# Kernel tuning notes

Measured on AMD Instinct MI355X. Metric: run time of the kernel, lower is better.

The kernel has to match this reference:

```python
import jax, jax.numpy as jnp
import numpy as np

N_NODES = 50000
N_EDGES = 800000


def gcn_layer(x, edge_index, W, b):
    """PyG-style GCNConv: add self-loops, symmetric deg^-1/2 normalization,
    linear transform, scatter-sum aggregation at target nodes, plus bias."""
    n = x.shape[0]
    loops = jnp.arange(n)
    src = jnp.concatenate([edge_index[0], loops])  # [E+N]
    dst = jnp.concatenate([edge_index[1], loops])  # [E+N]
    deg = jax.ops.segment_sum(jnp.ones(src.shape, dtype=x.dtype), dst, num_segments=n)
    dinv = jnp.where(deg > 0, jax.lax.rsqrt(deg), jnp.zeros((), x.dtype))
    norm = dinv[src] * dinv[dst]               # [E+N]
    h = x @ W                                   # [N, out]
    msg = norm[:, None] * h[src]                # [E+N, out] gather
    out = jax.ops.segment_sum(msg, dst, num_segments=n)  # scatter-add
    return out + b


def setup_inputs() -> dict:
    key = jax.random.key(0)
    ks = jax.random.split(key, 8)
    features = jax.random.normal(ks[0], (N_NODES, 64), dtype=jnp.float32)
    edge_index1 = jax.random.randint(ks[1], (2, N_EDGES), 0, N_NODES)
    edge_index3 = jax.random.randint(ks[2], (2, N_EDGES), 0, N_NODES)
    edge_index9 = jax.random.randint(ks[3], (2, N_EDGES), 0, N_NODES)

    def glorot(k, fi, fo):
        lim = float(np.sqrt(6.0 / (fi + fo)))
        return jax.random.uniform(k, (fi, fo), minval=-lim, maxval=lim, dtype=jnp.float32)

    W1 = glorot(ks[4], 64, 64)
    W2 = glorot(ks[5], 64, 32)
    W3 = glorot(ks[6], 32, 16)
    b1 = jnp.zeros((64,), jnp.float32)
    b2 = jnp.zeros((32,), jnp.float32)
    b3 = jnp.zeros((16,), jnp.float32)
    return dict(features=features, edge_index1=edge_index1, edge_index3=edge_index3,
                edge_index9=edge_index9, W1=W1, b1=b1, W2=W2, b2=b2, W3=W3, b3=b3)


def reference(features, edge_index1, edge_index3, edge_index9, W1, b1, W2, b2, W3, b3):
    x = jax.nn.relu(gcn_layer(features, edge_index1, W1, b1))  # hop 1
    x = jax.nn.relu(gcn_layer(x, edge_index3, W2, b2))         # hop 3
    x = jax.nn.relu(gcn_layer(x, edge_index9, W3, b3))         # hop 9
    return x
```

## Files before the change

kernel.cpp:

```cpp
#include <hip/hip_runtime.h>
#include <hip/hip_fp16.h>


#define NB   256
#define NL   3
#define TB   (NB * NL)
#define CAPE 6400
#define CAPE_E (CAPE + 8)
#define CH   4096
#define P1T  256
#define EPT  (CH / P1T)
#define P2T  512

__device__ __forceinline__ void decode_chunk(int g, int nc1, int nc2,
                                             const int* s1, const int* d1, int E1,
                                             const int* s2, const int* d2, int E2,
                                             const int* s3, const int* d3, int E3,
                                             const int** src, const int** dst, int* E, int* l,
                                             int* gout) {
    if (g < nc1)            { *src = s1; *dst = d1; *E = E1; *l = 0; }
    else if (g < nc1 + nc2) { *src = s2; *dst = d2; *E = E2; *l = 1; g -= nc1; }
    else                    { *src = s3; *dst = d3; *E = E3; *l = 2; g -= nc1 + nc2; }
    *gout = g;
}

__device__ __forceinline__ void fma4(float4& a, float s, const float4& w) {
    a.x += s * w.x; a.y += s * w.y; a.z += s * w.z; a.w += s * w.w;
}
__device__ __forceinline__ void add4(float4& a, const float4& v) {
    a.x += v.x; a.y += v.y; a.z += v.z; a.w += v.w;
}
__device__ __forceinline__ float4 ldh4(const __half* h, size_t idx4) {
    uint2 r = ((const uint2*)h)[idx4];
    __half2 a = *reinterpret_cast<__half2*>(&r.x);
    __half2 b = *reinterpret_cast<__half2*>(&r.y);
    float2 fa = __half22float2(a), fb = __half22float2(b);
    return make_float4(fa.x, fa.y, fb.x, fb.y);
}
__device__ __forceinline__ void sth4(__half* h, size_t idx4, float4 v) {
    __half2 a = __floats2half2_rn(v.x, v.y);
    __half2 b = __floats2half2_rn(v.z, v.w);
    uint2 r;
    r.x = *reinterpret_cast<unsigned*>(&a);
    r.y = *reinterpret_cast<unsigned*>(&b);
    ((uint2*)h)[idx4] = r;
}

__device__ __forceinline__ int wave_incl_scan(int v) {
    int incl = v;
#pragma unroll
    for (int off = 1; off < 64; off <<= 1) {
        int u = __shfl_up(incl, (unsigned)off, 64);
        if ((threadIdx.x & 63) >= off) incl += u;
    }
    return incl;
}

__global__ void __launch_bounds__(P1T) k1_phase1_gemm1(
        const int* __restrict__ s1, const int* __restrict__ d1, int E1,
        const int* __restrict__ s2, const int* __restrict__ d2, int E2,
        const int* __restrict__ s3, const int* __restrict__ d3, int E3,
        int nc1, int nc2, int W, int nchunks,
        int* __restrict__ gcur, unsigned int* __restrict__ pairBuf,
        const float* __restrict__ x0, const float* __restrict__ W1g,
        __half* __restrict__ h1) {
    __shared__ __align__(16) char smem[24576];
    __shared__ int wsum[4];
    const int t = threadIdx.x;
    if (blockIdx.x < (unsigned)nchunks) {
        int* hist = (int*)smem;
        int* eofs = hist + NB;
        int* bo   = eofs + NB;
        int* lcur = bo + NB;
        unsigned* stage = (unsigned*)(smem + 4096);
        unsigned char* stageQ = (unsigned char*)(smem + 20480);
        hist[t] = 0;
        __syncthreads();
        const int* src; const int* dst; int E, l, g;
        decode_chunk(blockIdx.x, nc1, nc2, s1, d1, E1, s2, d2, E2, s3, d3, E3,
                     &src, &dst, &E, &l, &g);
        const int e0 = g * CH;
        const int lbase = l * NB;
        unsigned pv[EPT];
        int bn[EPT];
        if (E - e0 >= CH) {
            const int4* s4 = (const int4*)(src + e0);
            const int4* d4 = (const int4*)(dst + e0);
#pragma unroll
            for (int w = 0; w < EPT / 4; ++w) {
                int4 sv = s4[t + w * P1T];
                int4 dv = d4[t + w * P1T];
                int q, i = w * 4;
                q = dv.x / W; bn[i+0] = q; pv[i+0] = ((unsigned)sv.x << 9) | (unsigned)(dv.x - q * W);
                q = dv.y / W; bn[i+1] = q; pv[i+1] = ((unsigned)sv.y << 9) | (unsigned)(dv.y - q * W);
                q = dv.z / W; bn[i+2] = q; pv[i+2] = ((unsigned)sv.z << 9) | (unsigned)(dv.z - q * W);
                q = dv.w / W; bn[i+3] = q; pv[i+3] = ((unsigned)sv.w << 9) | (unsigned)(dv.w - q * W);
            }
        } else {
#pragma unroll
            for (int i = 0; i < EPT; ++i) {
                int e = e0 + t + i * P1T;
                if (e < E) {
                    int s = src[e], d = dst[e];
                    int q = d / W;
                    bn[i] = q;
                    pv[i] = ((unsigned)s << 9) | (unsigned)(d - q * W);
                } else bn[i] = -1;
            }
        }
#pragma unroll
        for (int i = 0; i < EPT; ++i)
            if (bn[i] >= 0) atomicAdd(&hist[bn[i]], 1);
        __syncthreads();
        const int c = hist[t];
        int incl = wave_incl_scan(c);
        const int lane = t & 63, wid = t >> 6;
        if (lane == 63) wsum[wid] = incl;
        __syncthreads();
        int base = 0, total = 0;
#pragma unroll
        for (int w = 0; w < 4; ++w) {
            int s = wsum[w];
            total += s;
            if (w < wid) base += s;
        }
        const int excl = base + incl - c;
        eofs[t] = excl;
        lcur[t] = excl;
        bo[t] = (lbase + t) * CAPE + (c ? atomicAdd(&gcur[lbase + t], c) : 0);
        __syncthreads();
#pragma unroll
        for (int i = 0; i < EPT; ++i) {
            if (bn[i] >= 0) {
                int r = atomicAdd(&lcur[bn[i]], 1);
                stage[r] = pv[i];
                stageQ[r] = (unsigned char)bn[i];
            }
        }
        __syncthreads();
        for (int i = t; i < total; i += P1T) {
            int q = stageQ[i];
            int k = bo[q] + (i - eofs[q]);
            if (k < (lbase + q + 1) * CAPE) pairBuf[k] = stage[i];
        }
    } else {
        float* Ws = (float*)smem;
        const int bid = blockIdx.x - nchunks;
        for (int i = t; i < 1024; i += P1T)
            ((float4*)Ws)[i] = ((const float4*)W1g)[i];
        __syncthreads();
        const int tc = t % 16;
        const int tr = t / 16;
        const int row0 = bid * 64 + tr * 4;
        const float4* x4 = (const float4*)x0;
        const float4* Ws4 = (const float4*)Ws;
        float4 acc[4];
#pragma unroll
        for (int r = 0; r < 4; ++r) acc[r] = make_float4(0.f, 0.f, 0.f, 0.f);
        int rowc[4];
#pragma unroll
        for (int r = 0; r < 4; ++r) rowc[r] = min(row0 + r, 49999);
        for (int k0 = 0; k0 < 64; k0 += 4) {
            float4 wv0 = Ws4[(k0 + 0) * 16 + tc];
            float4 wv1 = Ws4[(k0 + 1) * 16 + tc];
            float4 wv2 = Ws4[(k0 + 2) * 16 + tc];
            float4 wv3 = Ws4[(k0 + 3) * 16 + tc];
#pragma unroll
            for (int r = 0; r < 4; ++r) {
                float4 xv = x4[(size_t)rowc[r] * 16 + (k0 / 4)];
                fma4(acc[r], xv.x, wv0);
                fma4(acc[r], xv.y, wv1);
                fma4(acc[r], xv.z, wv2);
                fma4(acc[r], xv.w, wv3);
            }
        }
#pragma unroll
        for (int r = 0; r < 4; ++r) {
            int row = row0 + r;
            if (row < 50000) sth4(h1, (size_t)row * 16 + tc, acc[r]);
        }
    }
}

__global__ void __launch_bounds__(P2T) k2_phase2(
        const unsigned int* __restrict__ pairBuf, const int* __restrict__ gcur,
        int n, int W,
        int* __restrict__ row_ptr, int* __restrict__ cnt_g,
        float* __restrict__ dinv, unsigned short* __restrict__ eidx,
        __half* __restrict__ h1, int* __restrict__ perm) {
    __shared__ __align__(16) char smem[19456];
    __shared__ int wsum[8];
    int* lcnt  = (int*)smem;
    int* lscan = lcnt + P2T;
    unsigned short* stage = (unsigned short*)(lscan + P2T);
    float* dloc = (float*)(smem + 17408);
    const int bid = blockIdx.x;
    const int l = bid / NB, k = bid % NB;
    const int lo = k * W;
    const int hi = min(n, lo + W);
    const int Wn = hi - lo;
    const int segE = min(gcur[bid], CAPE);
    const size_t base  = (size_t)bid * CAPE;
    const int    baseE = bid * CAPE_E;
    const int t = threadIdx.x;
    const int lane = t & 63, wid = t >> 6;
    lcnt[t] = 0;
    __syncthreads();
    for (int i = t; i < segE; i += P2T)
        atomicAdd(&lcnt[pairBuf[base + i] & 511u], 1);
    __syncthreads();
    const int v = lcnt[t];
    const int vp = (v + 3) & ~3;
    int incl = wave_incl_scan(vp);
    if (lane == 63) wsum[wid] = incl;
    __syncthreads();
    int sbase = 0, segEp = 0;
#pragma unroll
    for (int w = 0; w < 8; ++w) {
        int s = wsum[w];
        segEp += s;
        if (w < wid) sbase += s;
    }
    const int pexcl = sbase + incl - vp;
    if (t < Wn) {
        int node = l * n + lo + t;
        row_ptr[node] = baseE + pexcl;
        cnt_g[node] = v;
        float dv = rsqrtf((float)v + 1.0f);
        dinv[node] = dv;
        dloc[t] = dv;
    }
    __syncthreads();
    lcnt[t] = pexcl;
    __syncthreads();
    const bool lds_ok = (segEp <= CAPE);
    for (int i = t; i < segE; i += P2T) {
        unsigned p = pairBuf[base + i];
        int pos = atomicAdd(&lcnt[p & 511u], 1);
        unsigned short s = (unsigned short)(p >> 9);
        if (lds_ok) stage[pos] = s;
        else if (pos < CAPE_E) eidx[baseE + pos] = s;
    }
    __syncthreads();
    if (lds_ok) {
        const int4* st4 = (const int4*)stage;
        int4* e4 = (int4*)(eidx + baseE);
        int m16 = (segEp + 7) >> 3;
        for (int i = t; i < m16; i += P2T) e4[i] = st4[i];
    }
    if (l == 0) {
        for (int i = t; i < Wn * 16; i += P2T) {
            int r = i >> 4, cc = i & 15;
            size_t idx = (size_t)(lo + r) * 16 + cc;
            float4 vv = ldh4(h1, idx);
            float s = dloc[r];
            vv.x *= s; vv.y *= s; vv.z *= s; vv.w *= s;
            sth4(h1, idx, vv);
        }
    }
    __syncthreads();
    lcnt[t] = 0;
    __syncthreads();
    int key = 0, myr = 0;
    if (t < Wn) {
        key = min(v, 511);
        myr = atomicAdd(&lcnt[key], 1);
    }
    __syncthreads();
    const int c2 = lcnt[t];
    int incl2 = wave_incl_scan(c2);
    if (lane == 63) wsum[wid] = incl2;
    __syncthreads();
    int base2 = 0;
#pragma unroll
    for (int w = 0; w < 8; ++w) {
        int s = wsum[w];
        if (w < wid) base2 += s;
    }
    lscan[t] = base2 + incl2 - c2;
    __syncthreads();
    if (t < Wn) perm[l * n + lo + lscan[key] + myr] = lo + t;
}

__global__ void __launch_bounds__(256) k3_gather1_gemm2(
        const int* __restrict__ row_ptr, const int* __restrict__ cnt,
        const unsigned short* __restrict__ eidx, const float* __restrict__ dinv1,
        const float* __restrict__ dinv2, const int* __restrict__ perm,
        const __half* __restrict__ h1, const float* __restrict__ b1,
        const float* __restrict__ W2g, __half* __restrict__ h2, int n) {
    __shared__ float xs[16 * 68];
    __shared__ float W2s[64 * 32];
    for (int i = threadIdx.x; i < 512; i += 256)
        ((float4*)W2s)[i] = ((const float4*)W2g)[i];
    const int ln = threadIdx.x >> 4;
    const int f4 = threadIdx.x & 15;
    const int gidx = blockIdx.x * 16 + ln;
    const int node = (gidx < n) ? perm[gidx] : 0;
    if (gidx < n) {
        const int beg = row_ptr[node];
        const int m = cnt[node];
        float4 a0 = make_float4(0.f, 0.f, 0.f, 0.f), a1 = a0, a2 = a0, a3 = a0;
        int j = 0;
        for (; j + 8 <= m; j += 8) {
            ushort4 e0 = *(const ushort4*)(eidx + beg + j);
            ushort4 e1 = *(const ushort4*)(eidx + beg + j + 4);
            add4(a0, ldh4(h1, (size_t)e0.x * 16 + f4));
            add4(a1, ldh4(h1, (size_t)e0.y * 16 + f4));
            add4(a2, ldh4(h1, (size_t)e0.z * 16 + f4));
            add4(a3, ldh4(h1, (size_t)e0.w * 16 + f4));
            add4(a0, ldh4(h1, (size_t)e1.x * 16 + f4));
            add4(a1, ldh4(h1, (size_t)e1.y * 16 + f4));
            add4(a2, ldh4(h1, (size_t)e1.z * 16 + f4));
            add4(a3, ldh4(h1, (size_t)e1.w * 16 + f4));
        }
        if (j + 4 <= m) {
            ushort4 e0 = *(const ushort4*)(eidx + beg + j);
            add4(a0, ldh4(h1, (size_t)e0.x * 16 + f4));
            add4(a1, ldh4(h1, (size_t)e0.y * 16 + f4));
            add4(a2, ldh4(h1, (size_t)e0.z * 16 + f4));
            add4(a3, ldh4(h1, (size_t)e0.w * 16 + f4));
            j += 4;
        }
        for (; j < m; ++j)
            add4(a0, ldh4(h1, (size_t)eidx[beg + j] * 16 + f4));
        add4(a0, a1); add4(a2, a3); add4(a0, a2);
        float di = dinv1[node];
        float4 self = ldh4(h1, (size_t)node * 16 + f4);
        float4 bv = ((const float4*)b1)[f4];
        float4 o;
        o.x = di * (a0.x + self.x) + bv.x;
        o.y = di * (a0.y + self.y) + bv.y;
        o.z = di * (a0.z + self.z) + bv.z;
        o.w = di * (a0.w + self.w) + bv.w;
        o.x = o.x > 0.f ? o.x : 0.f;
        o.y = o.y > 0.f ? o.y : 0.f;
        o.z = o.z > 0.f ? o.z : 0.f;
        o.w = o.w > 0.f ? o.w : 0.f;
        *(float4*)&xs[ln * 68 + f4 * 4] = o;
    }
    __syncthreads();
    if (gidx < n) {
        const int c0 = f4 * 2;
        float s0 = 0.f, s1 = 0.f;
#pragma unroll
        for (int k = 0; k < 64; ++k) {
            float xv = xs[ln * 68 + k];
            s0 += xv * W2s[k * 32 + c0];
            s1 += xv * W2s[k * 32 + c0 + 1];
        }
        float d2 = dinv2[node];
        ((__half2*)h2)[(size_t)node * 16 + f4] = __floats2half2_rn(s0 * d2, s1 * d2);
    }
}

__global__ void __launch_bounds__(256) k4_gather2_gemm3(
        const int* __restrict__ row_ptr2, const int* __restrict__ cnt2,
        const unsigned short* __restrict__ eidx, const float* __restrict__ dinv2,
        const float* __restrict__ dinv3, const int* __restrict__ perm,
        const __half* __restrict__ h2, const float* __restrict__ b2,
        const float* __restrict__ W3g, __half* __restrict__ h3, int n) {
    __shared__ float xs[32 * 36];
    __shared__ float W3s[32 * 16];
    for (int i = threadIdx.x; i < 128; i += 256)
        ((float4*)W3s)[i] = ((const float4*)W3g)[i];
    const int ln = threadIdx.x >> 3;
    const int f4 = threadIdx.x & 7;
    const int gidx = blockIdx.x * 32 + ln;
    const int node = (gidx < n) ? perm[gidx] : 0;
    if (gidx < n) {
        const int beg = row_ptr2[node];
        const int m = cnt2[node];
        float4 a0 = make_float4(0.f, 0.f, 0.f, 0.f), a1 = a0, a2 = a0, a3 = a0;
        int j = 0;
        for (; j + 8 <= m; j += 8) {
            ushort4 e0 = *(const ushort4*)(eidx + beg + j);
            ushort4 e1 = *(const ushort4*)(eidx + beg + j + 4);
            add4(a0, ldh4(h2, (size_t)e0.x * 8 + f4));
            add4(a1, ldh4(h2, (size_t)e0.y * 8 + f4));
            add4(a2, ldh4(h2, (size_t)e0.z * 8 + f4));
            add4(a3, ldh4(h2, (size_t)e0.w * 8 + f4));
            add4(a0, ldh4(h2, (size_t)e1.x * 8 + f4));
            add4(a1, ldh4(h2, (size_t)e1.y * 8 + f4));
            add4(a2, ldh4(h2, (size_t)e1.z * 8 + f4));
            add4(a3, ldh4(h2, (size_t)e1.w * 8 + f4));
        }
        if (j + 4 <= m) {
            ushort4 e0 = *(const ushort4*)(eidx + beg + j);
            add4(a0, ldh4(h2, (size_t)e0.x * 8 + f4));
            add4(a1, ldh4(h2, (size_t)e0.y * 8 + f4));
            add4(a2, ldh4(h2, (size_t)e0.z * 8 + f4));
            add4(a3, ldh4(h2, (size_t)e0.w * 8 + f4));
            j += 4;
        }
        for (; j < m; ++j)
            add4(a0, ldh4(h2, (size_t)eidx[beg + j] * 8 + f4));
        add4(a0, a1); add4(a2, a3); add4(a0, a2);
        float di = dinv2[node];
        float4 self = ldh4(h2, (size_t)node * 8 + f4);
        float4 bv = ((const float4*)b2)[f4];
        float4 o;
        o.x = di * (a0.x + self.x) + bv.x;
        o.y = di * (a0.y + self.y) + bv.y;
        o.z = di * (a0.z + self.z) + bv.z;
        o.w = di * (a0.w + self.w) + bv.w;
        o.x = o.x > 0.f ? o.x : 0.f;
        o.y = o.y > 0.f ? o.y : 0.f;
        o.z = o.z > 0.f ? o.z : 0.f;
        o.w = o.w > 0.f ? o.w : 0.f;
        *(float4*)&xs[ln * 36 + f4 * 4] = o;
    }
    __syncthreads();
    if (gidx < n) {
        const int c0 = f4 * 2;
        float s0 = 0.f, s1 = 0.f;
#pragma unroll
        for (int k = 0; k < 32; ++k) {
            float xv = xs[ln * 36 + k];
            s0 += xv * W3s[k * 16 + c0];
            s1 += xv * W3s[k * 16 + c0 + 1];
        }
        float d3 = dinv3[node];
        ((__half2*)h3)[(size_t)node * 8 + f4] = __floats2half2_rn(s0 * d3, s1 * d3);
    }
}

__global__ void __launch_bounds__(256) k5_gather3(
        const int* __restrict__ row_ptr3, const int* __restrict__ cnt3,
        const unsigned short* __restrict__ eidx, const float* __restrict__ dinv3,
        const int* __restrict__ perm,
        const __half* __restrict__ h3, const float* __restrict__ b3,
        float* __restrict__ out, int n) {
    const int ln = threadIdx.x >> 2;
    const int f4 = threadIdx.x & 3;
    const int gidx = blockIdx.x * 64 + ln;
    if (gidx >= n) return;
    const int node = perm[gidx];
    const int beg = row_ptr3[node];
    const int m = cnt3[node];
    float4 a0 = make_float4(0.f, 0.f, 0.f, 0.f), a1 = a0, a2 = a0, a3 = a0;
    int j = 0;
    for (; j + 8 <= m; j += 8) {
        ushort4 e0 = *(const ushort4*)(eidx + beg + j);
        ushort4 e1 = *(const ushort4*)(eidx + beg + j + 4);
        add4(a0, ldh4(h3, (size_t)e0.x * 4 + f4));
        add4(a1, ldh4(h3, (size_t)e0.y * 4 + f4));
        add4(a2, ldh4(h3, (size_t)e0.z * 4 + f4));
        add4(a3, ldh4(h3, (size_t)e0.w * 4 + f4));
        add4(a0, ldh4(h3, (size_t)e1.x * 4 + f4));
        add4(a1, ldh4(h3, (size_t)e1.y * 4 + f4));
        add4(a2, ldh4(h3, (size_t)e1.z * 4 + f4));
        add4(a3, ldh4(h3, (size_t)e1.w * 4 + f4));
    }
    if (j + 4 <= m) {
        ushort4 e0 = *(const ushort4*)(eidx + beg + j);
        add4(a0, ldh4(h3, (size_t)e0.x * 4 + f4));
        add4(a1, ldh4(h3, (size_t)e0.y * 4 + f4));
        add4(a2, ldh4(h3, (size_t)e0.z * 4 + f4));
        add4(a3, ldh4(h3, (size_t)e0.w * 4 + f4));
        j += 4;
    }
    for (; j < m; ++j)
        add4(a0, ldh4(h3, (size_t)eidx[beg + j] * 4 + f4));
    add4(a0, a1); add4(a2, a3); add4(a0, a2);
    float di = dinv3[node];
    float4 self = ldh4(h3, (size_t)node * 4 + f4);
    float4 bv = ((const float4*)b3)[f4];
    float4 o;
    o.x = di * (a0.x + self.x) + bv.x;
    o.y = di * (a0.y + self.y) + bv.y;
    o.z = di * (a0.z + self.z) + bv.z;
    o.w = di * (a0.w + self.w) + bv.w;
    o.x = o.x > 0.f ? o.x : 0.f;
    o.y = o.y > 0.f ? o.y : 0.f;
    o.z = o.z > 0.f ? o.z : 0.f;
    o.w = o.w > 0.f ? o.w : 0.f;
    ((float4*)out)[(size_t)node * 4 + f4] = o;
}

extern "C" void kernel_launch(void* const* d_in, const int* in_sizes, int n_in,
                              void* d_out, int out_size, void* d_ws, size_t ws_size,
                              hipStream_t stream) {
    const float* x0  = (const float*)d_in[0];
    const int*   ei1 = (const int*)d_in[1];
    const int*   ei3 = (const int*)d_in[2];
    const int*   ei9 = (const int*)d_in[3];
    const float* W1  = (const float*)d_in[4];
    const float* b1  = (const float*)d_in[5];
    const float* W2  = (const float*)d_in[6];
    const float* b2  = (const float*)d_in[7];
    const float* W3  = (const float*)d_in[8];
    const float* b3  = (const float*)d_in[9];

    const int n  = in_sizes[0] / 64;
    const int E1 = in_sizes[1] / 2;
    const int E3 = in_sizes[2] / 2;
    const int E9 = in_sizes[3] / 2;
    const int n3 = 3 * n;
    const int W  = (n + NB - 1) / NB;

    const int nc1 = (E1 + CH - 1) / CH;
    const int nc2 = (E3 + CH - 1) / CH;
    const int nc3 = (E9 + CH - 1) / CH;
    const int nchunks = nc1 + nc2 + nc3;
    const int gemmBlks = (n + 63) / 64;

    int* gcur    = (int*)d_ws;
    unsigned int* pairBuf = (unsigned int*)(gcur + TB);
    unsigned short* eidx = (unsigned short*)(pairBuf + (size_t)TB * CAPE);
    int* row_ptr = (int*)(eidx + (size_t)TB * CAPE_E);
    int* cnt     = row_ptr + n3;
    float* dinv  = (float*)(cnt + n3);
    int* perm    = (int*)(dinv + n3);
    __half* h1   = (__half*)(perm + n3);
    __half* h2   = h1 + (size_t)n * 64;
    __half* h3   = h2 + (size_t)n * 32;

    hipMemsetAsync(gcur, 0, TB * sizeof(int), stream);
    k1_phase1_gemm1<<<nchunks + gemmBlks, P1T, 0, stream>>>(
        ei1, ei1 + E1, E1, ei3, ei3 + E3, E3, ei9, ei9 + E9, E9,
        nc1, nc2, W, nchunks, gcur, pairBuf, x0, W1, h1);
    k2_phase2<<<TB, P2T, 0, stream>>>(
        pairBuf, gcur, n, W, row_ptr, cnt, dinv, eidx, h1, perm);
    k3_gather1_gemm2<<<(n + 15) / 16, 256, 0, stream>>>(
        row_ptr, cnt, eidx, dinv, dinv + n, perm, h1, b1, W2, h2, n);
    k4_gather2_gemm3<<<(n + 31) / 32, 256, 0, stream>>>(
        row_ptr + n, cnt + n, eidx, dinv + n, dinv + 2 * n, perm + n, h2, b2, W3, h3, n);
    k5_gather3<<<(n + 63) / 64, 256, 0, stream>>>(
        row_ptr + 2 * n, cnt + 2 * n, eidx, dinv + 2 * n, perm + 2 * n, h3, b3, (float*)d_out, n);
}
```

Baseline: 158.6 us.

## Fuse five kernels into one persistent kernel with grid-wide barriers

Replaces the five launches (bucketing+GEMM1, CSR build, and three gather layers) with a single persistent kernel of 768 blocks that loops over work units and separates phases with atomic-counter grid barriers. It also halves the edge chunk size and moves phase 2 from 512 to 256 threads. The aim is to remove per-launch overhead and inter-kernel gaps. In exchange it depends on all 768 blocks being co-resident, since otherwise the barrier deadlocks, and it pays spin-wait cost plus reduced parallelism in the phases that previously used more blocks.

```diff
diff --git a/kernel.cpp b/kernel.cpp
--- a/kernel.cpp
+++ b/kernel.cpp
@@ -7,10 +7,10 @@
 #define TB   (NB * NL)
 #define CAPE 6400
 #define CAPE_E (CAPE + 8)
-#define CH   4096
-#define P1T  256
-#define EPT  (CH / P1T)
-#define P2T  512
+#define CH   2048
+#define PT   256
+#define EPT  (CH / PT)
+#define GRID 768
 
 __device__ __forceinline__ void decode_chunk(int g, int nc1, int nc2,
                                              const int* s1, const int* d1, int E1,
@@ -56,425 +56,447 @@
     return incl;
 }
 
-__global__ void __launch_bounds__(P1T) k1_phase1_gemm1(
+__device__ __forceinline__ void gbar(int* bar, int idx) {
+    __syncthreads();
+    if (threadIdx.x == 0) {
+        __threadfence();
+        __hip_atomic_fetch_add(&bar[idx], 1, __ATOMIC_ACQ_REL, __HIP_MEMORY_SCOPE_AGENT);
+        while (__hip_atomic_load(&bar[idx], __ATOMIC_RELAXED, __HIP_MEMORY_SCOPE_AGENT) < GRID)
+            __builtin_amdgcn_s_sleep(1);
+        __threadfence();
+    }
+    __syncthreads();
+}
+
+__global__ void __launch_bounds__(PT, 4) mega(
         const int* __restrict__ s1, const int* __restrict__ d1, int E1,
         const int* __restrict__ s2, const int* __restrict__ d2, int E2,
         const int* __restrict__ s3, const int* __restrict__ d3, int E3,
-        int nc1, int nc2, int W, int nchunks,
-        int* __restrict__ gcur, unsigned int* __restrict__ pairBuf,
+        int nc1, int nc2, int W, int nchunks, int gemmBlks, int n,
+        int* __restrict__ gcur, int* __restrict__ bar,
+        unsigned int* __restrict__ pairBuf, unsigned short* __restrict__ eidx,
+        int* __restrict__ row_ptr, int* __restrict__ cnt_g,
+        float* __restrict__ dinv, int* __restrict__ perm,
         const float* __restrict__ x0, const float* __restrict__ W1g,
-        __half* __restrict__ h1) {
-    __shared__ __align__(16) char smem[24576];
+        const float* __restrict__ b1, const float* __restrict__ W2g,
+        const float* __restrict__ b2, const float* __restrict__ W3g,
+        const float* __restrict__ b3,
+        __half* __restrict__ h1, __half* __restrict__ h2, __half* __restrict__ h3,
+        float* __restrict__ out) {
+    __shared__ __align__(16) char smem[17408];
     __shared__ int wsum[4];
     const int t = threadIdx.x;
-    if (blockIdx.x < (unsigned)nchunks) {
-        int* hist = (int*)smem;
-        int* eofs = hist + NB;
-        int* bo   = eofs + NB;
-        int* lcur = bo + NB;
-        unsigned* stage = (unsigned*)(smem + 4096);
-        unsigned char* stageQ = (unsigned char*)(smem + 20480);
-        hist[t] = 0;
-        __syncthreads();
-        const int* src; const int* dst; int E, l, g;
-        decode_chunk(blockIdx.x, nc1, nc2, s1, d1, E1, s2, d2, E2, s3, d3, E3,
-                     &src, &dst, &E, &l, &g);
-        const int e0 = g * CH;
-        const int lbase = l * NB;
-        unsigned pv[EPT];
-        int bn[EPT];
-        if (E - e0 >= CH) {
-            const int4* s4 = (const int4*)(src + e0);
-            const int4* d4 = (const int4*)(dst + e0);
-#pragma unroll
-            for (int w = 0; w < EPT / 4; ++w) {
-                int4 sv = s4[t + w * P1T];
-                int4 dv = d4[t + w * P1T];
-                int q, i = w * 4;
-                q = dv.x / W; bn[i+0] = q; pv[i+0] = ((unsigned)sv.x << 9) | (unsigned)(dv.x - q * W);
-                q = dv.y / W; bn[i+1] = q; pv[i+1] = ((unsigned)sv.y << 9) | (unsigned)(dv.y - q * W);
-                q = dv.z / W; bn[i+2] = q; pv[i+2] = ((unsigned)sv.z << 9) | (unsigned)(dv.z - q * W);
-                q = dv.w / W; bn[i+3] = q; pv[i+3] = ((unsigned)sv.w << 9) | (unsigned)(dv.w - q * W);
+    const int bid = blockIdx.x;
+    const int lane = t & 63, wid = t >> 6;
+
+    for (int u = bid; u < nchunks + gemmBlks; u += GRID) {
+        if (u < nchunks) {
+            int* hist = (int*)smem;
+            int* eofs = hist + NB;
+            int* bo   = eofs + NB;
+            int* lcur = bo + NB;
+            unsigned* stage = (unsigned*)(smem + 4096);
+            unsigned char* stageQ = (unsigned char*)(smem + 12288);
+            hist[t] = 0;
+            __syncthreads();
+            const int* src; const int* dst; int E, l, g;
+            decode_chunk(u, nc1, nc2, s1, d1, E1, s2, d2, E2, s3, d3, E3,
+                         &src, &dst, &E, &l, &g);
+            const int e0 = g * CH;
+            const int lbase = l * NB;
+            unsigned pv[EPT];
+            int bn[EPT];
+            if (E - e0 >= CH) {
+                const int4* s4 = (const int4*)(src + e0);
+                const int4* d4 = (const int4*)(dst + e0);
+#pragma unroll
+                for (int w = 0; w < EPT / 4; ++w) {
+                    int4 sv = s4[t + w * PT];
+                    int4 dv = d4[t + w * PT];
+                    int q, i = w * 4;
+                    q = dv.x / W; bn[i+0] = q; pv[i+0] = ((unsigned)sv.x << 9) | (unsigned)(dv.x - q * W);
+                    q = dv.y / W; bn[i+1] = q; pv[i+1] = ((unsigned)sv.y << 9) | (unsigned)(dv.y - q * W);
+                    q = dv.z / W; bn[i+2] = q; pv[i+2] = ((unsigned)sv.z << 9) | (unsigned)(dv.z - q * W);
+                    q = dv.w / W; bn[i+3] = q; pv[i+3] = ((unsigned)sv.w << 9) | (unsigned)(dv.w - q * W);
+                }
+            } else {
+#pragma unroll
+                for (int i = 0; i < EPT; ++i) {
+                    int e = e0 + t + i * PT;
+                    if (e < E) {
+                        int s = src[e], d = dst[e];
+                        int q = d / W;
+                        bn[i] = q;
+                        pv[i] = ((unsigned)s << 9) | (unsigned)(d - q * W);
+                    } else bn[i] = -1;
+                }
+            }
+#pragma unroll
+            for (int i = 0; i < EPT; ++i)
+                if (bn[i] >= 0) atomicAdd(&hist[bn[i]], 1);
+            __syncthreads();
+            const int c = hist[t];
+            int incl = wave_incl_scan(c);
+            if (lane == 63) wsum[wid] = incl;
+            __syncthreads();
+            int base = 0, total = 0;
+#pragma unroll
+            for (int w = 0; w < 4; ++w) {
+                int s = wsum[w];
+                total += s;
+                if (w < wid) base += s;
+            }
+            const int excl = base + incl - c;
+            eofs[t] = excl;
+            lcur[t] = excl;
+            bo[t] = (lbase + t) * CAPE + (c ? atomicAdd(&gcur[lbase + t], c) : 0);
+            __syncthreads();
+#pragma unroll
+            for (int i = 0; i < EPT; ++i) {
+                if (bn[i] >= 0) {
+                    int r = atomicAdd(&lcur[bn[i]], 1);
+                    stage[r] = pv[i];
+                    stageQ[r] = (unsigned char)bn[i];
+                }
+            }
+            __syncthreads();
+            for (int i = t; i < total; i += PT) {
+                int q = stageQ[i];
+                int k = bo[q] + (i - eofs[q]);
+                if (k < (lbase + q + 1) * CAPE) pairBuf[k] = stage[i];
             }
         } else {
-#pragma unroll
-            for (int i = 0; i < EPT; ++i) {
-                int e = e0 + t + i * P1T;
-                if (e < E) {
-                    int s = src[e], d = dst[e];
-                    int q = d / W;
-                    bn[i] = q;
-                    pv[i] = ((unsigned)s << 9) | (unsigned)(d - q * W);
-                } else bn[i] = -1;
-            }
-        }
-#pragma unroll
-        for (int i = 0; i < EPT; ++i)
-            if (bn[i] >= 0) atomicAdd(&hist[bn[i]], 1);
-        __syncthreads();
-        const int c = hist[t];
-        int incl = wave_incl_scan(c);
-        const int lane = t & 63, wid = t >> 6;
+            float* Ws = (float*)smem;
+            const int gb = u - nchunks;
+            for (int i = t; i < 1024; i += PT)
+                ((float4*)Ws)[i] = ((const float4*)W1g)[i];
+            __syncthreads();
+            const int tc = t % 16;
+            const int tr = t / 16;
+            const int row0 = gb * 64 + tr * 4;
+            const float4* x4 = (const float4*)x0;
+            const float4* Ws4 = (const float4*)Ws;
+            float4 acc[4];
+#pragma unroll
+            for (int r = 0; r < 4; ++r) acc[r] = make_float4(0.f, 0.f, 0.f, 0.f);
+            int rowc[4];
+#pragma unroll
+            for (int r = 0; r < 4; ++r) rowc[r] = min(row0 + r, n - 1);
+            for (int k0 = 0; k0 < 64; k0 += 4) {
+                float4 wv0 = Ws4[(k0 + 0) * 16 + tc];
+                float4 wv1 = Ws4[(k0 + 1) * 16 + tc];
+                float4 wv2 = Ws4[(k0 + 2) * 16 + tc];
+                float4 wv3 = Ws4[(k0 + 3) * 16 + tc];
+#pragma unroll
+                for (int r = 0; r < 4; ++r) {
+                    float4 xv = x4[(size_t)rowc[r] * 16 + (k0 / 4)];
+                    fma4(acc[r], xv.x, wv0);
+                    fma4(acc[r], xv.y, wv1);
+                    fma4(acc[r], xv.z, wv2);
+                    fma4(acc[r], xv.w, wv3);
+                }
+            }
+#pragma unroll
+            for (int r = 0; r < 4; ++r) {
+                int row = row0 + r;
+                if (row < n) sth4(h1, (size_t)row * 16 + tc, acc[r]);
+            }
+        }
+        __syncthreads();
+    }
+    gbar(bar, 0);
+
+    for (int u = bid; u < TB; u += GRID) {
+        int* lcnt  = (int*)smem;
+        int* lscan = (int*)(smem + 1024);
+        unsigned short* stage = (unsigned short*)(smem + 2048);
+        float* dloc = (float*)(smem + 14848);
+        const int l = u / NB, k2 = u % NB;
+        const int lo = k2 * W;
+        const int hi = min(n, lo + W);
+        const int Wn = hi - lo;
+        const int segE = min(gcur[u], CAPE);
+        const size_t base  = (size_t)u * CAPE;
+        const int    baseE = u * CAPE_E;
+        lcnt[t] = 0;
+        __syncthreads();
+        for (int i = t; i < segE; i += PT)
+            atomicAdd(&lcnt[pairBuf[base + i] & 511u], 1);
+        __syncthreads();
+        const int v = lcnt[t];
+        const int vp = (v + 3) & ~3;
+        int incl = wave_incl_scan(vp);
         if (lane == 63) wsum[wid] = incl;
         __syncthreads();
-        int base = 0, total = 0;
+        int sbase = 0, segEp = 0;
 #pragma unroll
         for (int w = 0; w < 4; ++w) {
             int s = wsum[w];
-            total += s;
-            if (w < wid) base += s;
-        }
-        const int excl = base + incl - c;
-        eofs[t] = excl;
-        lcur[t] = excl;
-        bo[t] = (lbase + t) * CAPE + (c ? atomicAdd(&gcur[lbase + t], c) : 0);
-        __syncthreads();
-#pragma unroll
-        for (int i = 0; i < EPT; ++i) {
-            if (bn[i] >= 0) {
-                int r = atomicAdd(&lcur[bn[i]], 1);
-                stage[r] = pv[i];
-                stageQ[r] = (unsigned char)bn[i];
-            }
-        }
-        __syncthreads();
-        for (int i = t; i < total; i += P1T) {
-            int q = stageQ[i];
-            int k = bo[q] + (i - eofs[q]);
-            if (k < (lbase + q + 1) * CAPE) pairBuf[k] = stage[i];
-        }
-    } else {
-        float* Ws = (float*)smem;
-        const int bid = blockIdx.x - nchunks;
-        for (int i = t; i < 1024; i += P1T)
-            ((float4*)Ws)[i] = ((const float4*)W1g)[i];
-        __syncthreads();
-        const int tc = t % 16;
-        const int tr = t / 16;
-        const int row0 = bid * 64 + tr * 4;
-        const float4* x4 = (const float4*)x0;
-        const float4* Ws4 = (const float4*)Ws;
-        float4 acc[4];
-#pragma unroll
-        for (int r = 0; r < 4; ++r) acc[r] = make_float4(0.f, 0.f, 0.f, 0.f);
-        int rowc[4];
-#pragma unroll
-        for (int r = 0; r < 4; ++r) rowc[r] = min(row0 + r, 49999);
-        for (int k0 = 0; k0 < 64; k0 += 4) {
-            float4 wv0 = Ws4[(k0 + 0) * 16 + tc];
-            float4 wv1 = Ws4[(k0 + 1) * 16 + tc];
-            float4 wv2 = Ws4[(k0 + 2) * 16 + tc];
-            float4 wv3 = Ws4[(k0 + 3) * 16 + tc];
-#pragma unroll
-            for (int r = 0; r < 4; ++r) {
-                float4 xv = x4[(size_t)rowc[r] * 16 + (k0 / 4)];
-                fma4(acc[r], xv.x, wv0);
-                fma4(acc[r], xv.y, wv1);
-                fma4(acc[r], xv.z, wv2);
-                fma4(acc[r], xv.w, wv3);
-            }
-        }
-#pragma unroll
-        for (int r = 0; r < 4; ++r) {
-            int row = row0 + r;
-            if (row < 50000) sth4(h1, (size_t)row * 16 + tc, acc[r]);
-        }
-    }
-}
-
-__global__ void __launch_bounds__(P2T) k2_phase2(
-        const unsigned int* __restrict__ pairBuf, const int* __restrict__ gcur,
-        int n, int W,
-        int* __restrict__ row_ptr, int* __restrict__ cnt_g,
-        float* __restrict__ dinv, unsigned short* __restrict__ eidx,
-        __half* __restrict__ h1, int* __restrict__ perm) {
-    __shared__ __align__(16) char smem[19456];
-    __shared__ int wsum[8];
-    int* lcnt  = (int*)smem;
-    int* lscan = lcnt + P2T;
-    unsigned short* stage = (unsigned short*)(lscan + P2T);
-    float* dloc = (float*)(smem + 17408);
-    const int bid = blockIdx.x;
-    const int l = bid / NB, k = bid % NB;
-    const int lo = k * W;
-    const int hi = min(n, lo + W);
-    const int Wn = hi - lo;
-    const int segE = min(gcur[bid], CAPE);
-    const size_t base  = (size_t)bid * CAPE;
-    const int    baseE = bid * CAPE_E;
-    const int t = threadIdx.x;
-    const int lane = t & 63, wid = t >> 6;
-    lcnt[t] = 0;
-    __syncthreads();
-    for (int i = t; i < segE; i += P2T)
-        atomicAdd(&lcnt[pairBuf[base + i] & 511u], 1);
-    __syncthreads();
-    const int v = lcnt[t];
-    const int vp = (v + 3) & ~3;
-    int incl = wave_incl_scan(vp);
-    if (lane == 63) wsum[wid] = incl;
-    __syncthreads();
-    int sbase = 0, segEp = 0;
-#pragma unroll
-    for (int w = 0; w < 8; ++w) {
-        int s = wsum[w];
-        segEp += s;
-        if (w < wid) sbase += s;
-    }
-    const int pexcl = sbase + incl - vp;
-    if (t < Wn) {
-        int node = l * n + lo + t;
-        row_ptr[node] = baseE + pexcl;
-        cnt_g[node] = v;
-        float dv = rsqrtf((float)v + 1.0f);
-        dinv[node] = dv;
-        dloc[t] = dv;
-    }
-    __syncthreads();
-    lcnt[t] = pexcl;
-    __syncthreads();
-    const bool lds_ok = (segEp <= CAPE);
-    for (int i = t; i < segE; i += P2T) {
-        unsigned p = pairBuf[base + i];
-        int pos = atomicAdd(&lcnt[p & 511u], 1);
-        unsigned short s = (unsigned short)(p >> 9);
-        if (lds_ok) stage[pos] = s;
-        else if (pos < CAPE_E) eidx[baseE + pos] = s;
-    }
-    __syncthreads();
-    if (lds_ok) {
-        const int4* st4 = (const int4*)stage;
-        int4* e4 = (int4*)(eidx + baseE);
-        int m16 = (segEp + 7) >> 3;
-        for (int i = t; i < m16; i += P2T) e4[i] = st4[i];
-    }
-    if (l == 0) {
-        for (int i = t; i < Wn * 16; i += P2T) {
-            int r = i >> 4, cc = i & 15;
-            size_t idx = (size_t)(lo + r) * 16 + cc;
-            float4 vv = ldh4(h1, idx);
-            float s = dloc[r];
-            vv.x *= s; vv.y *= s; vv.z *= s; vv.w *= s;
-            sth4(h1, idx, vv);
-        }
-    }
-    __syncthreads();
-    lcnt[t] = 0;
-    __syncthreads();
-    int key = 0, myr = 0;
-    if (t < Wn) {
-        key = min(v, 511);
-        myr = atomicAdd(&lcnt[key], 1);
-    }
-    __syncthreads();
-    const int c2 = lcnt[t];
-    int incl2 = wave_incl_scan(c2);
-    if (lane == 63) wsum[wid] = incl2;
-    __syncthreads();
-    int base2 = 0;
-#pragma unroll
-    for (int w = 0; w < 8; ++w) {
-        int s = wsum[w];
-        if (w < wid) base2 += s;
-    }
-    lscan[t] = base2 + incl2 - c2;
-    __syncthreads();
-    if (t < Wn) perm[l * n + lo + lscan[key] + myr] = lo + t;
-}
-
-__global__ void __launch_bounds__(256) k3_gather1_gemm2(
-        const int* __restrict__ row_ptr, const int* __restrict__ cnt,
-        const unsigned short* __restrict__ eidx, const float* __restrict__ dinv1,
-        const float* __restrict__ dinv2, const int* __restrict__ perm,
-        const __half* __restrict__ h1, const float* __restrict__ b1,
-        const float* __restrict__ W2g, __half* __restrict__ h2, int n) {
-    __shared__ float xs[16 * 68];
-    __shared__ float W2s[64 * 32];
-    for (int i = threadIdx.x; i < 512; i += 256)
-        ((float4*)W2s)[i] = ((const float4*)W2g)[i];
-    const int ln = threadIdx.x >> 4;
-    const int f4 = threadIdx.x & 15;
-    const int gidx = blockIdx.x * 16 + ln;
-    const int node = (gidx < n) ? perm[gidx] : 0;
-    if (gidx < n) {
-        const int beg = row_ptr[node];
-        const int m = cnt[node];
-        float4 a0 = make_float4(0.f, 0.f, 0.f, 0.f), a1 = a0, a2 = a0, a3 = a0;
-        int j = 0;
-        for (; j + 8 <= m; j += 8) {
-            ushort4 e0 = *(const ushort4*)(eidx + beg + j);
-            ushort4 e1 = *(const ushort4*)(eidx + beg + j + 4);
-            add4(a0, ldh4(h1, (size_t)e0.x * 16 + f4));
-            add4(a1, ldh4(h1, (size_t)e0.y * 16 + f4));
-            add4(a2, ldh4(h1, (size_t)e0.z * 16 + f4));
-            add4(a3, ldh4(h1, (size_t)e0.w * 16 + f4));
-            add4(a0, ldh4(h1, (size_t)e1.x * 16 + f4));
-            add4(a1, ldh4(h1, (size_t)e1.y * 16 + f4));
-            add4(a2, ldh4(h1, (size_t)e1.z * 16 + f4));
-            add4(a3, ldh4(h1, (size_t)e1.w * 16 + f4));
-        }
-        if (j + 4 <= m) {
-            ushort4 e0 = *(const ushort4*)(eidx + beg + j);
-            add4(a0, ldh4(h1, (size_t)e0.x * 16 + f4));
-            add4(a1, ldh4(h1, (size_t)e0.y * 16 + f4));
-            add4(a2, ldh4(h1, (size_t)e0.z * 16 + f4));
-            add4(a3, ldh4(h1, (size_t)e0.w * 16 + f4));
-            j += 4;
-        }
-        for (; j < m; ++j)
-            add4(a0, ldh4(h1, (size_t)eidx[beg + j] * 16 + f4));
-        add4(a0, a1); add4(a2, a3); add4(a0, a2);
-        float di = dinv1[node];
-        float4 self = ldh4(h1, (size_t)node * 16 + f4);
-        float4 bv = ((const float4*)b1)[f4];
-        float4 o;
-        o.x = di * (a0.x + self.x) + bv.x;
-        o.y = di * (a0.y + self.y) + bv.y;
-        o.z = di * (a0.z + self.z) + bv.z;
-        o.w = di * (a0.w + self.w) + bv.w;
-        o.x = o.x > 0.f ? o.x : 0.f;
-        o.y = o.y > 0.f ? o.y : 0.f;
-        o.z = o.z > 0.f ? o.z : 0.f;
-        o.w = o.w > 0.f ? o.w : 0.f;
-        *(float4*)&xs[ln * 68 + f4 * 4] = o;
-    }
-    __syncthreads();
-    if (gidx < n) {
-        const int c0 = f4 * 2;
-        float s0 = 0.f, s1 = 0.f;
-#pragma unroll
-        for (int k = 0; k < 64; ++k) {
-            float xv = xs[ln * 68 + k];
-            s0 += xv * W2s[k * 32 + c0];
-            s1 += xv * W2s[k * 32 + c0 + 1];
-        }
-        float d2 = dinv2[node];
-        ((__half2*)h2)[(size_t)node * 16 + f4] = __floats2half2_rn(s0 * d2, s1 * d2);
-    }
-}
-
-__global__ void __launch_bounds__(256) k4_gather2_gemm3(
-        const int* __restrict__ row_ptr2, const int* __restrict__ cnt2,
-        const unsigned short* __restrict__ eidx, const float* __restrict__ dinv2,
-        const float* __restrict__ dinv3, const int* __restrict__ perm,
-        const __half* __restrict__ h2, const float* __restrict__ b2,
-        const float* __restrict__ W3g, __half* __restrict__ h3, int n) {
-    __shared__ float xs[32 * 36];
-    __shared__ float W3s[32 * 16];
-    for (int i = threadIdx.x; i < 128; i += 256)
-        ((float4*)W3s)[i] = ((const float4*)W3g)[i];
-    const int ln = threadIdx.x >> 3;
-    const int f4 = threadIdx.x & 7;
-    const int gidx = blockIdx.x * 32 + ln;
-    const int node = (gidx < n) ? perm[gidx] : 0;
-    if (gidx < n) {
-        const int beg = row_ptr2[node];
-        const int m = cnt2[node];
-        float4 a0 = make_float4(0.f, 0.f, 0.f, 0.f), a1 = a0, a2 = a0, a3 = a0;
-        int j = 0;
-        for (; j + 8 <= m; j += 8) {
-            ushort4 e0 = *(const ushort4*)(eidx + beg + j);
-            ushort4 e1 = *(const ushort4*)(eidx + beg + j + 4);
-            add4(a0, ldh4(h2, (size_t)e0.x * 8 + f4));
-            add4(a1, ldh4(h2, (size_t)e0.y * 8 + f4));
-            add4(a2, ldh4(h2, (size_t)e0.z * 8 + f4));
-            add4(a3, ldh4(h2, (size_t)e0.w * 8 + f4));
-            add4(a0, ldh4(h2, (size_t)e1.x * 8 + f4));
-            add4(a1, ldh4(h2, (size_t)e1.y * 8 + f4));
-            add4(a2, ldh4(h2, (size_t)e1.z * 8 + f4));
-            add4(a3, ldh4(h2, (size_t)e1.w * 8 + f4));
-        }
-        if (j + 4 <= m) {
-            ushort4 e0 = *(const ushort4*)(eidx + beg + j);
-            add4(a0, ldh4(h2, (size_t)e0.x * 8 + f4));
-            add4(a1, ldh4(h2, (size_t)e0.y * 8 + f4));
-            add4(a2, ldh4(h2, (size_t)e0.z * 8 + f4));
-            add4(a3, ldh4(h2, (size_t)e0.w * 8 + f4));
-            j += 4;
-        }
-        for (; j < m; ++j)
-            add4(a0, ldh4(h2, (size_t)eidx[beg + j] * 8 + f4));
-        add4(a0, a1); add4(a2, a3); add4(a0, a2);
-        float di = dinv2[node];
-        float4 self = ldh4(h2, (size_t)node * 8 + f4);
-        float4 bv = ((const float4*)b2)[f4];
-        float4 o;
-        o.x = di * (a0.x + self.x) + bv.x;
-        o.y = di * (a0.y + self.y) + bv.y;
-        o.z = di * (a0.z + self.z) + bv.z;
-        o.w = di * (a0.w + self.w) + bv.w;
-        o.x = o.x > 0.f ? o.x : 0.f;
-        o.y = o.y > 0.f ? o.y : 0.f;
-        o.z = o.z > 0.f ? o.z : 0.f;
-        o.w = o.w > 0.f ? o.w : 0.f;
-        *(float4*)&xs[ln * 36 + f4 * 4] = o;
-    }
-    __syncthreads();
-    if (gidx < n) {
-        const int c0 = f4 * 2;
-        float s0 = 0.f, s1 = 0.f;
-#pragma unroll
-        for (int k = 0; k < 32; ++k) {
-            float xv = xs[ln * 36 + k];
-            s0 += xv * W3s[k * 16 + c0];
-            s1 += xv * W3s[k * 16 + c0 + 1];
-        }
-        float d3 = dinv3[node];
-        ((__half2*)h3)[(size_t)node * 8 + f4] = __floats2half2_rn(s0 * d3, s1 * d3);
-    }
-}
-
-__global__ void __launch_bounds__(256) k5_gather3(
-        const int* __restrict__ row_ptr3, const int* __restrict__ cnt3,
-        const unsigned short* __restrict__ eidx, const float* __restrict__ dinv3,
-        const int* __restrict__ perm,
-        const __half* __restrict__ h3, const float* __restrict__ b3,
-        float* __restrict__ out, int n) {
-    const int ln = threadIdx.x >> 2;
-    const int f4 = threadIdx.x & 3;
-    const int gidx = blockIdx.x * 64 + ln;
-    if (gidx >= n) return;
-    const int node = perm[gidx];
-    const int beg = row_ptr3[node];
-    const int m = cnt3[node];
-    float4 a0 = make_float4(0.f, 0.f, 0.f, 0.f), a1 = a0, a2 = a0, a3 = a0;
-    int j = 0;
-    for (; j + 8 <= m; j += 8) {
-        ushort4 e0 = *(const ushort4*)(eidx + beg + j);
-        ushort4 e1 = *(const ushort4*)(eidx + beg + j + 4);
-        add4(a0, ldh4(h3, (size_t)e0.x * 4 + f4));
-        add4(a1, ldh4(h3, (size_t)e0.y * 4 + f4));
-        add4(a2, ldh4(h3, (size_t)e0.z * 4 + f4));
-        add4(a3, ldh4(h3, (size_t)e0.w * 4 + f4));
-        add4(a0, ldh4(h3, (size_t)e1.x * 4 + f4));
-        add4(a1, ldh4(h3, (size_t)e1.y * 4 + f4));
-        add4(a2, ldh4(h3, (size_t)e1.z * 4 + f4));
-        add4(a3, ldh4(h3, (size_t)e1.w * 4 + f4));
-    }
-    if (j + 4 <= m) {
-        ushort4 e0 = *(const ushort4*)(eidx + beg + j);
-        add4(a0, ldh4(h3, (size_t)e0.x * 4 + f4));
-        add4(a1, ldh4(h3, (size_t)e0.y * 4 + f4));
-        add4(a2, ldh4(h3, (size_t)e0.z * 4 + f4));
-        add4(a3, ldh4(h3, (size_t)e0.w * 4 + f4));
-        j += 4;
-    }
-    for (; j < m; ++j)
-        add4(a0, ldh4(h3, (size_t)eidx[beg + j] * 4 + f4));
-    add4(a0, a1); add4(a2, a3); add4(a0, a2);
-    float di = dinv3[node];
-    float4 self = ldh4(h3, (size_t)node * 4 + f4);
-    float4 bv = ((const float4*)b3)[f4];
-    float4 o;
-    o.x = di * (a0.x + self.x) + bv.x;
-    o.y = di * (a0.y + self.y) + bv.y;
-    o.z = di * (a0.z + self.z) + bv.z;
-    o.w = di * (a0.w + self.w) + bv.w;
-    o.x = o.x > 0.f ? o.x : 0.f;
-    o.y = o.y > 0.f ? o.y : 0.f;
-    o.z = o.z > 0.f ? o.z : 0.f;
-    o.w = o.w > 0.f ? o.w : 0.f;
-    ((float4*)out)[(size_t)node * 4 + f4] = o;
+            segEp += s;
+            if (w < wid) sbase += s;
+        }
+        const int pexcl = sbase + incl - vp;
+        if (t < Wn) {
+            int node = l * n + lo + t;
+            row_ptr[node] = baseE + pexcl;
+            cnt_g[node] = v;
+            float dv = rsqrtf((float)v + 1.0f);
+            dinv[node] = dv;
+            dloc[t] = dv;
+        }
+        __syncthreads();
+        lcnt[t] = pexcl;
+        __syncthreads();
+        const bool lds_ok = (segEp <= CAPE);
+        for (int i = t; i < segE; i += PT) {
+            unsigned p = pairBuf[base + i];
+            int pos = atomicAdd(&lcnt[p & 511u], 1);
+            unsigned short s = (unsigned short)(p >> 9);
+            if (lds_ok) stage[pos] = s;
+            else if (pos < CAPE_E) eidx[baseE + pos] = s;
+        }
+        __syncthreads();
+        if (lds_ok) {
+            const int4* st4 = (const int4*)stage;
+            int4* e4 = (int4*)(eidx + baseE);
+            int m16 = (segEp + 7) >> 3;
+            for (int i = t; i < m16; i += PT) e4[i] = st4[i];
+        }
+        if (l == 0) {
+            for (int i = t; i < Wn * 16; i += PT) {
+                int r = i >> 4, cc = i & 15;
+                size_t idx = (size_t)(lo + r) * 16 + cc;
+                float4 vv = ldh4(h1, idx);
+                float s = dloc[r];
+                vv.x *= s; vv.y *= s; vv.z *= s; vv.w *= s;
+                sth4(h1, idx, vv);
+            }
+        }
+        __syncthreads();
+        lcnt[t] = 0;
+        __syncthreads();
+        int key = 0, myr = 0;
+        if (t < Wn) {
+            key = min(v, 255);
+            myr = atomicAdd(&lcnt[key], 1);
+        }
+        __syncthreads();
+        const int c2 = lcnt[t];
+        int incl2 = wave_incl_scan(c2);
+        if (lane == 63) wsum[wid] = incl2;
+        __syncthreads();
+        int base2 = 0;
+#pragma unroll
+        for (int w = 0; w < 4; ++w)
+            if (w < wid) base2 += wsum[w];
+        lscan[t] = base2 + incl2 - c2;
+        __syncthreads();
+        if (t < Wn) perm[l * n + lo + lscan[key] + myr] = lo + t;
+        __syncthreads();
+    }
+    gbar(bar, 1);
+
+    {
+        float* W2s = (float*)smem;
+        float* xs  = (float*)(smem + 8192);
+        for (int i = t; i < 512; i += PT)
+            ((float4*)W2s)[i] = ((const float4*)W2g)[i];
+        __syncthreads();
+        const int ln = t >> 4;
+        const int f4 = t & 15;
+        const int nu = (n + 15) / 16;
+        for (int u = bid; u < nu; u += GRID) {
+            const int gidx = u * 16 + ln;
+            const int node = (gidx < n) ? perm[gidx] : 0;
+            if (gidx < n) {
+                const int beg = row_ptr[node];
+                const int m = cnt_g[node];
+                float4 a0 = make_float4(0.f, 0.f, 0.f, 0.f), a1 = a0, a2 = a0, a3 = a0;
+                int j = 0;
+                for (; j + 8 <= m; j += 8) {
+                    ushort4 e0 = *(const ushort4*)(eidx + beg + j);
+                    ushort4 e1 = *(const ushort4*)(eidx + beg + j + 4);
+                    add4(a0, ldh4(h1, (size_t)e0.x * 16 + f4));
+                    add4(a1, ldh4(h1, (size_t)e0.y * 16 + f4));
+                    add4(a2, ldh4(h1, (size_t)e0.z * 16 + f4));
+                    add4(a3, ldh4(h1, (size_t)e0.w * 16 + f4));
+                    add4(a0, ldh4(h1, (size_t)e1.x * 16 + f4));
+                    add4(a1, ldh4(h1, (size_t)e1.y * 16 + f4));
+                    add4(a2, ldh4(h1, (size_t)e1.z * 16 + f4));
+                    add4(a3, ldh4(h1, (size_t)e1.w * 16 + f4));
+                }
+                if (j + 4 <= m) {
+                    ushort4 e0 = *(const ushort4*)(eidx + beg + j);
+                    add4(a0, ldh4(h1, (size_t)e0.x * 16 + f4));
+                    add4(a1, ldh4(h1, (size_t)e0.y * 16 + f4));
+                    add4(a2, ldh4(h1, (size_t)e0.z * 16 + f4));
+                    add4(a3, ldh4(h1, (size_t)e0.w * 16 + f4));
+                    j += 4;
+                }
+                for (; j < m; ++j)
+                    add4(a0, ldh4(h1, (size_t)eidx[beg + j] * 16 + f4));
+                add4(a0, a1); add4(a2, a3); add4(a0, a2);
+                float di = dinv[node];
+                float4 self = ldh4(h1, (size_t)node * 16 + f4);
+                float4 bv = ((const float4*)b1)[f4];
+                float4 o;
+                o.x = di * (a0.x + self.x) + bv.x;
+                o.y = di * (a0.y + self.y) + bv.y;
+                o.z = di * (a0.z + self.z) + bv.z;
+                o.w = di * (a0.w + self.w) + bv.w;
+                o.x = o.x > 0.f ? o.x : 0.f;
+                o.y = o.y > 0.f ? o.y : 0.f;
+                o.z = o.z > 0.f ? o.z : 0.f;
+                o.w = o.w > 0.f ? o.w : 0.f;
+                *(float4*)&xs[ln * 68 + f4 * 4] = o;
+            }
+            __syncthreads();
+            if (gidx < n) {
+                const int c0 = f4 * 2;
+                float s0 = 0.f, s1 = 0.f;
+#pragma unroll
+                for (int k = 0; k < 64; ++k) {
+                    float xv = xs[ln * 68 + k];
+                    s0 += xv * W2s[k * 32 + c0];
+                    s1 += xv * W2s[k * 32 + c0 + 1];
+                }
+                float d2 = dinv[n + node];
+                ((__half2*)h2)[(size_t)node * 16 + f4] = __floats2half2_rn(s0 * d2, s1 * d2);
+            }
+            __syncthreads();
+        }
+    }
+    gbar(bar, 2);
+
+    {
+        float* W3s = (float*)smem;
+        float* xs  = (float*)(smem + 2048);
+        for (int i = t; i < 128; i += PT)
+            ((float4*)W3s)[i] = ((const float4*)W3g)[i];
+        __syncthreads();
+        const int ln = t >> 3;
+        const int f4 = t & 7;
+        const int nu = (n + 31) / 32;
+        const int* rp2 = row_ptr + n;
+        const int* ct2 = cnt_g + n;
+        const int* pm2 = perm + n;
+        for (int u = bid; u < nu; u += GRID) {
+            const int gidx = u * 32 + ln;
+            const int node = (gidx < n) ? pm2[gidx] : 0;
+            if (gidx < n) {
+                const int beg = rp2[node];
+                const int m = ct2[node];
+                float4 a0 = make_float4(0.f, 0.f, 0.f, 0.f), a1 = a0, a2 = a0, a3 = a0;
+                int j = 0;
+                for (; j + 8 <= m; j += 8) {
+                    ushort4 e0 = *(const ushort4*)(eidx + beg + j);
+                    ushort4 e1 = *(const ushort4*)(eidx + beg + j + 4);
+                    add4(a0, ldh4(h2, (size_t)e0.x * 8 + f4));
+                    add4(a1, ldh4(h2, (size_t)e0.y * 8 + f4));
+                    add4(a2, ldh4(h2, (size_t)e0.z * 8 + f4));
+                    add4(a3, ldh4(h2, (size_t)e0.w * 8 + f4));
+                    add4(a0, ldh4(h2, (size_t)e1.x * 8 + f4));
+                    add4(a1, ldh4(h2, (size_t)e1.y * 8 + f4));
+                    add4(a2, ldh4(h2, (size_t)e1.z * 8 + f4));
+                    add4(a3, ldh4(h2, (size_t)e1.w * 8 + f4));
+                }
+                if (j + 4 <= m) {
+                    ushort4 e0 = *(const ushort4*)(eidx + beg + j);
+                    add4(a0, ldh4(h2, (size_t)e0.x * 8 + f4));
+                    add4(a1, ldh4(h2, (size_t)e0.y * 8 + f4));
+                    add4(a2, ldh4(h2, (size_t)e0.z * 8 + f4));
+                    add4(a3, ldh4(h2, (size_t)e0.w * 8 + f4));
+                    j += 4;
+                }
+                for (; j < m; ++j)
+                    add4(a0, ldh4(h2, (size_t)eidx[beg + j] * 8 + f4));
+                add4(a0, a1); add4(a2, a3); add4(a0, a2);
+                float di = dinv[n + node];
+                float4 self = ldh4(h2, (size_t)node * 8 + f4);
+                float4 bv = ((const float4*)b2)[f4];
+                float4 o;
+                o.x = di * (a0.x + self.x) + bv.x;
+                o.y = di * (a0.y + self.y) + bv.y;
+                o.z = di * (a0.z + self.z) + bv.z;
+                o.w = di * (a0.w + self.w) + bv.w;
+                o.x = o.x > 0.f ? o.x : 0.f;
+                o.y = o.y > 0.f ? o.y : 0.f;
+                o.z = o.z > 0.f ? o.z : 0.f;
+                o.w = o.w > 0.f ? o.w : 0.f;
+                *(float4*)&xs[ln * 36 + f4 * 4] = o;
+            }
+            __syncthreads();
+            if (gidx < n) {
+                const int c0 = f4 * 2;
+                float s0 = 0.f, s1 = 0.f;
+#pragma unroll
+                for (int k = 0; k < 32; ++k) {
+                    float xv = xs[ln * 36 + k];
+                    s0 += xv * W3s[k * 16 + c0];
+                    s1 += xv * W3s[k * 16 + c0 + 1];
+                }
+                float d3 = dinv[2 * n + node];
+                ((__half2*)h3)[(size_t)node * 8 + f4] = __floats2half2_rn(s0 * d3, s1 * d3);
+            }
+            __syncthreads();
+        }
+    }
+    gbar(bar, 3);
+
+    {
+        const int ln = t >> 2;
+        const int f4 = t & 3;
+        const int nu = (n + 63) / 64;
+        const int* rp3 = row_ptr + 2 * n;
+        const int* ct3 = cnt_g + 2 * n;
+        const int* pm3 = perm + 2 * n;
+        const float* dv3 = dinv + 2 * n;
+        for (int u = bid; u < nu; u += GRID) {
+            const int gidx = u * 64 + ln;
+            if (gidx >= n) continue;
+            const int node = pm3[gidx];
+            const int beg = rp3[node];
+            const int m = ct3[node];
+            float4 a0 = make_float4(0.f, 0.f, 0.f, 0.f), a1 = a0, a2 = a0, a3 = a0;
+            int j = 0;
+            for (; j + 8 <= m; j += 8) {
+                ushort4 e0 = *(const ushort4*)(eidx + beg + j);
+                ushort4 e1 = *(const ushort4*)(eidx + beg + j + 4);
+                add4(a0, ldh4(h3, (size_t)e0.x * 4 + f4));
+                add4(a1, ldh4(h3, (size_t)e0.y * 4 + f4));
+                add4(a2, ldh4(h3, (size_t)e0.z * 4 + f4));
+                add4(a3, ldh4(h3, (size_t)e0.w * 4 + f4));
+                add4(a0, ldh4(h3, (size_t)e1.x * 4 + f4));
+                add4(a1, ldh4(h3, (size_t)e1.y * 4 + f4));
+                add4(a2, ldh4(h3, (size_t)e1.z * 4 + f4));
+                add4(a3, ldh4(h3, (size_t)e1.w * 4 + f4));
+            }
+            if (j + 4 <= m) {
+                ushort4 e0 = *(const ushort4*)(eidx + beg + j);
+                add4(a0, ldh4(h3, (size_t)e0.x * 4 + f4));
+                add4(a1, ldh4(h3, (size_t)e0.y * 4 + f4));
+                add4(a2, ldh4(h3, (size_t)e0.z * 4 + f4));
+                add4(a3, ldh4(h3, (size_t)e0.w * 4 + f4));
+                j += 4;
+            }
+            for (; j < m; ++j)
+                add4(a0, ldh4(h3, (size_t)eidx[beg + j] * 4 + f4));
+            add4(a0, a1); add4(a2, a3); add4(a0, a2);
+            float di = dv3[node];
+            float4 self = ldh4(h3, (size_t)node * 4 + f4);
+            float4 bv = ((const float4*)b3)[f4];
+            float4 o;
+            o.x = di * (a0.x + self.x) + bv.x;
+            o.y = di * (a0.y + self.y) + bv.y;
+            o.z = di * (a0.z + self.z) + bv.z;
+            o.w = di * (a0.w + self.w) + bv.w;
+            o.x = o.x > 0.f ? o.x : 0.f;
+            o.y = o.y > 0.f ? o.y : 0.f;
+            o.z = o.z > 0.f ? o.z : 0.f;
+            o.w = o.w > 0.f ? o.w : 0.f;
+            ((float4*)out)[(size_t)node * 4 + f4] = o;
+        }
+    }
 }
 
 extern "C" void kernel_launch(void* const* d_in, const int* in_sizes, int n_in,
@@ -505,7 +527,8 @@
     const int gemmBlks = (n + 63) / 64;
 
     int* gcur    = (int*)d_ws;
-    unsigned int* pairBuf = (unsigned int*)(gcur + TB);
+    int* bar     = gcur + TB;
+    unsigned int* pairBuf = (unsigned int*)(bar + 8);
     unsigned short* eidx = (unsigned short*)(pairBuf + (size_t)TB * CAPE);
     int* row_ptr = (int*)(eidx + (size_t)TB * CAPE_E);
     int* cnt     = row_ptr + n3;
@@ -515,16 +538,10 @@
     __half* h2   = h1 + (size_t)n * 64;
     __half* h3   = h2 + (size_t)n * 32;
 
-    hipMemsetAsync(gcur, 0, TB * sizeof(int), stream);
-    k1_phase1_gemm1<<<nchunks + gemmBlks, P1T, 0, stream>>>(
+    hipMemsetAsync(gcur, 0, (TB + 8) * sizeof(int), stream);
+    mega<<<GRID, PT, 0, stream>>>(
         ei1, ei1 + E1, E1, ei3, ei3 + E3, E3, ei9, ei9 + E9, E9,
-        nc1, nc2, W, nchunks, gcur, pairBuf, x0, W1, h1);
-    k2_phase2<<<TB, P2T, 0, stream>>>(
-        pairBuf, gcur, n, W, row_ptr, cnt, dinv, eidx, h1, perm);
-    k3_gather1_gemm2<<<(n + 15) / 16, 256, 0, stream>>>(
-        row_ptr, cnt, eidx, dinv, dinv + n, perm, h1, b1, W2, h2, n);
-    k4_gather2_gemm3<<<(n + 31) / 32, 256, 0, stream>>>(
-        row_ptr + n, cnt + n, eidx, dinv + n, dinv + 2 * n, perm + n, h2, b2, W3, h3, n);
-    k5_gather3<<<(n + 63) / 64, 256, 0, stream>>>(
-        row_ptr + 2 * n, cnt + 2 * n, eidx, dinv + 2 * n, perm + 2 * n, h3, b3, (float*)d_out, n);
-}
+        nc1, nc2, W, nchunks, gemmBlks, n,
+        gcur, bar, pairBuf, eidx, row_ptr, cnt, dinv, perm,
+        x0, W1, b1, W2, b2, W3, b3, h1, h2, h3, (float*)d_out);
+}
```

Result: slower. 614.6 us (+287.5%).
